# Performance work log

Hardware: AMD Instinct MI355X
Metric: run time of the kernel (lower is better)

The kernel has to match this reference:

```python
import jax, jax.numpy as jnp
import numpy as np

B, S, D = 4, 2048, 1024
H = 16
DK = D // H  # 64


def setup_inputs() -> dict:
    key = jax.random.key(0)
    k1, k2, k3 = jax.random.split(key, 3)
    std_qkv = (2.0 / (D + 3 * D)) ** 0.5
    std_o = (2.0 / (D + D)) ** 0.5
    x = jax.random.normal(k1, (B, S, D), dtype=jnp.float32)
    W_qkv = jax.random.normal(k2, (3 * D, D), dtype=jnp.float32) * std_qkv
    W_o = jax.random.normal(k3, (D, D), dtype=jnp.float32) * std_o
    return {"x": x, "W_qkv": W_qkv, "W_o": W_o}


def reference(x, W_qkv, W_o):
    b, s, d = x.shape
    # qkv projection: [b, s, 3*H*DK]
    qkv = jnp.einsum('bsd,ed->bse', x, W_qkv)
    # rearrange '(c h dk)' -> c, b, h, s, dk
    qkv = qkv.reshape(b, s, 3, H, DK)
    qkv = jnp.transpose(qkv, (2, 0, 3, 1, 4))  # [3, b, h, s, dk]
    q, k, v = qkv[0], qkv[1], qkv[2]
    # scaled dot product attention with causal mask
    scores = jnp.einsum('bhqd,bhkd->bhqk', q, k) / (DK ** 0.5)
    causal = jnp.tril(jnp.ones((s, s), dtype=bool))
    scores = jnp.where(causal, scores, -jnp.inf)
    probs = jax.nn.softmax(scores, axis=-1)
    heads = jnp.einsum('bhqk,bhkd->bhqd', probs, v)
    # merge heads: [b, s, H*DK]
    heads = jnp.transpose(heads, (0, 2, 1, 3)).reshape(b, s, H * DK)
    return jnp.einsum('bse,de->bsd', heads, W_o)
```

## Files before the change

kernel.cpp:

```cpp
#include <hip/hip_runtime.h>
#include <hip/hip_bf16.h>

#define BB 4
#define SS 2048
#define DD 1024
#define HH 16
#define DKK 64

typedef __bf16 bf16x8 __attribute__((ext_vector_type(8)));
typedef float floatx4 __attribute__((ext_vector_type(4)));

#if __has_builtin(__builtin_amdgcn_exp2f)
#define EXP2(x) __builtin_amdgcn_exp2f(x)
#else
#define EXP2(x) exp2f(x)
#endif

__device__ __forceinline__ float b2f(unsigned short u) {
    union { unsigned int i; float f; } c;
    c.i = ((unsigned int)u) << 16;
    return c.f;
}
__device__ __forceinline__ unsigned short f2b(float f) {
    unsigned int i = __float_as_uint(f);
    unsigned int r = (i + 0x7FFFu + ((i >> 16) & 1u)) >> 16;
    return (unsigned short)r;
}

__device__ __forceinline__ void gload_lds16(const unsigned short* g,
                                            unsigned short* l) {
    __builtin_amdgcn_global_load_lds(
        (const __attribute__((address_space(1))) unsigned int*)g,
        (__attribute__((address_space(3))) unsigned int*)l, 16, 0, 0);
}

__global__ void cvt_f32_bf16(const float* __restrict__ in,
                             unsigned short* __restrict__ out, int n4) {
    int i = blockIdx.x * blockDim.x + threadIdx.x;
    if (i >= n4) return;
    float4 v = ((const float4*)in)[i];
    ushort4 o;
    o.x = f2b(v.x); o.y = f2b(v.y); o.z = f2b(v.z); o.w = f2b(v.w);
    ((ushort4*)out)[i] = o;
}

template <typename CT>
__global__ void gemm_nt_lds(const unsigned short* __restrict__ A,
                            const unsigned short* __restrict__ B,
                            CT* __restrict__ C, int M, int N, int K) {
    __shared__ unsigned short Alds[128][32];
    __shared__ unsigned short Blds[128][32];

    const int tid  = threadIdx.x;
    const int lane = tid & 63;
    const int w    = tid >> 6;
    const int wm   = (w & 1) * 64;
    const int wn   = (w >> 1) * 64;

    const int m0 = blockIdx.x * 128;
    const int n0 = blockIdx.y * 128;

    const int row16 = lane & 15;
    const int part  = lane >> 4;
    const int rbase = part * 4;

    const int srow = lane >> 2;
    const int scol = (lane & 3) * 8;

    const unsigned short* Ag = A + (size_t)(m0 + w * 16 + srow) * K + scol;
    const unsigned short* Bg = B + (size_t)(n0 + w * 16 + srow) * K + scol;
    unsigned short* Al = &Alds[w * 16][0];
    unsigned short* Bl = &Blds[w * 16][0];
    const size_t rstep = (size_t)64 * K;

    floatx4 acc[4][4] = {};

    for (int k0 = 0; k0 < K; k0 += 32) {
        __syncthreads();
        gload_lds16(Ag + k0,         Al);
        gload_lds16(Ag + rstep + k0, Al + 64 * 32);
        gload_lds16(Bg + k0,         Bl);
        gload_lds16(Bg + rstep + k0, Bl + 64 * 32);
        __syncthreads();

        bf16x8 af[4], bfr[4];
#pragma unroll
        for (int i = 0; i < 4; ++i)
            af[i] = *(const bf16x8*)&Alds[wm + i * 16 + row16][part * 8];
#pragma unroll
        for (int j = 0; j < 4; ++j)
            bfr[j] = *(const bf16x8*)&Blds[wn + j * 16 + row16][part * 8];
#pragma unroll
        for (int i = 0; i < 4; ++i)
#pragma unroll
            for (int j = 0; j < 4; ++j)
                acc[i][j] = __builtin_amdgcn_mfma_f32_16x16x32_bf16(
                    af[i], bfr[j], acc[i][j], 0, 0, 0);
    }

#pragma unroll
    for (int i = 0; i < 4; ++i) {
#pragma unroll
        for (int j = 0; j < 4; ++j) {
            const int row = m0 + wm + i * 16 + rbase;
            const int col = n0 + wn + j * 16 + row16;
#pragma unroll
            for (int r = 0; r < 4; ++r) {
                size_t idx = (size_t)(row + r) * N + col;
                if constexpr (sizeof(CT) == 2) C[idx] = f2b(acc[i][j][r]);
                else                           C[idx] = acc[i][j][r];
            }
        }
    }
}

__global__ void repack_kv(const unsigned short* __restrict__ qkv,
                          unsigned short* __restrict__ Kp,
                          unsigned short* __restrict__ Vt) {
    __shared__ unsigned short Vs[64][72];
    const int st = blockIdx.x, h = blockIdx.y, b = blockIdx.z;
    const int tid = threadIdx.x;
    const size_t base = ((size_t)((b * HH + h) * (SS / 64) + st)) * 4096;

#pragma unroll
    for (int p = 0; p < 2; ++p) {
        const int row = p * 32 + (tid >> 3);
        const int chunk = tid & 7;
        size_t src = (size_t)(b * SS + st * 64 + row) * (3 * DD) +
                     DD + h * DKK + chunk * 8;
        uint4 kv = *(const uint4*)(qkv + src);
        *(uint4*)(Kp + base + (chunk >> 2) * 2048 + row * 32 + (chunk & 3) * 8) = kv;
        uint4 vv = *(const uint4*)(qkv + src + DD);
        *(uint4*)&Vs[row][chunk * 8] = vv;
    }
    __syncthreads();
#pragma unroll
    for (int p = 0; p < 2; ++p) {
        const int dk = p * 32 + (tid >> 3);
        const int s8 = tid & 7;
        union { unsigned short u[8]; uint4 v; } pk;
#pragma unroll
        for (int j = 0; j < 8; ++j) pk.u[j] = Vs[s8 * 8 + j][dk];
        *(uint4*)(Vt + base + (s8 >> 2) * 2048 + dk * 32 + (s8 & 3) * 8) = pk.v;
    }
}

__global__ __launch_bounds__(256) void attn_mfma5(
    const unsigned short* __restrict__ qkv,
    const unsigned short* __restrict__ Kp,
    const unsigned short* __restrict__ Vt,
    unsigned short* __restrict__ heads) {
    const int tid  = threadIdx.x;
    const int lane = tid & 63;
    const int w    = tid >> 6;

    const int u0   = blockIdx.x;
    const int xcd  = u0 & 7;
    const int slot = u0 >> 3;
    const int pair = xcd * 8 + (slot >> 4);
    const int qx   = 15 - (slot & 15);
    const int b = pair >> 4, h = pair & 15;
    const int q0w = qx * 128 + w * 32;

    const int row16 = lane & 15;
    const int part  = lane >> 4;
    const int rbase = part * 4;
    const float c1 = 0.180336884f;

    bf16x8 qf[2][2];
#pragma unroll
    for (int qt = 0; qt < 2; ++qt)
#pragma unroll
        for (int u = 0; u < 2; ++u) {
            const unsigned short* qp = qkv +
                (size_t)(b * SS + q0w + qt * 16 + row16) * (3 * DD) +
                h * DKK + u * 32 + part * 8;
            union { uint4 r; unsigned short us[8]; } raw;
            raw.r = *(const uint4*)qp;
            union { unsigned short us[8]; bf16x8 v; } sq;
#pragma unroll
            for (int j = 0; j < 8; ++j) sq.us[j] = f2b(b2f(raw.us[j]) * c1);
            qf[qt][u] = sq.v;
        }

    floatx4 O[2][4] = {};
    float mrow[2] = {-1e30f, -1e30f}, lrow[2] = {0.f, 0.f};

    const size_t tb = (size_t)pair * (SS / 64) * 4096;
    const int ntiles = (q0w + 31) / 64 + 1;

    for (int t = 0; t < ntiles; ++t) {
        const int k0 = t * 64;
        const unsigned short* kbase = Kp + tb + (size_t)t * 4096;
        const unsigned short* vbase = Vt + tb + (size_t)t * 4096;
        bf16x8 kf[2][4], vf[2][4];
#pragma unroll
        for (int u = 0; u < 2; ++u)
#pragma unroll
            for (int i = 0; i < 4; ++i) {
                kf[u][i] = *(const bf16x8*)(kbase + u * 2048 +
                                            (i * 16 + row16) * 32 + part * 8);
                vf[u][i] = *(const bf16x8*)(vbase + u * 2048 +
                                            (i * 16 + row16) * 32 + part * 8);
            }

#pragma unroll
        for (int qt = 0; qt < 2; ++qt) {
            floatx4 sc[4] = {};
#pragma unroll
            for (int u = 0; u < 2; ++u)
#pragma unroll
                for (int kt = 0; kt < 4; ++kt)
                    sc[kt] = __builtin_amdgcn_mfma_f32_16x16x32_bf16(
                        kf[u][kt], qf[qt][u], sc[kt], 0, 0, 0);

            const int qa = q0w + qt * 16 + row16;
            const bool full = (k0 + 63 <= q0w + qt * 16);
            float mx = -1e30f;
#pragma unroll
            for (int kt = 0; kt < 4; ++kt)
#pragma unroll
                for (int r = 0; r < 4; ++r) {
                    float s = sc[kt][r];
                    if (!full) {
                        int ka = k0 + kt * 16 + rbase + r;
                        s = (ka <= qa) ? s : -1e30f;
                    }
                    sc[kt][r] = s;
                    mx = fmaxf(mx, s);
                }
            mx = fmaxf(mx, __shfl_xor(mx, 16));
            mx = fmaxf(mx, __shfl_xor(mx, 32));
            float mnew = fmaxf(mrow[qt], mx);
            float alpha = EXP2(mrow[qt] - mnew);

            float ps = 0.f;
            unsigned int pk[4][2];
#pragma unroll
            for (int kt = 0; kt < 4; ++kt) {
                float e0 = EXP2(sc[kt][0] - mnew);
                float e1 = EXP2(sc[kt][1] - mnew);
                float e2 = EXP2(sc[kt][2] - mnew);
                float e3 = EXP2(sc[kt][3] - mnew);
                ps += (e0 + e1) + (e2 + e3);
                pk[kt][0] = (unsigned int)f2b(e0) | ((unsigned int)f2b(e1) << 16);
                pk[kt][1] = (unsigned int)f2b(e2) | ((unsigned int)f2b(e3) << 16);
            }
            ps += __shfl_xor(ps, 16);
            ps += __shfl_xor(ps, 32);
            lrow[qt] = lrow[qt] * alpha + ps;
            mrow[qt] = mnew;

#pragma unroll
            for (int dt = 0; dt < 4; ++dt) O[qt][dt] *= alpha;

            const int l0 = row16 + ((part & 1) * 2 + 0) * 16;
            const int l1 = row16 + ((part & 1) * 2 + 1) * 16;
            const bool hi = (part >> 1);
#pragma unroll
            for (int u = 0; u < 2; ++u) {
                unsigned int lo00 = (unsigned int)__shfl((int)pk[2 * u][0], l0);
                unsigned int lo01 = (unsigned int)__shfl((int)pk[2 * u][1], l0);
                unsigned int lo10 = (unsigned int)__shfl((int)pk[2 * u][0], l1);
                unsigned int lo11 = (unsigned int)__shfl((int)pk[2 * u][1], l1);
                unsigned int hi00 = (unsigned int)__shfl((int)pk[2 * u + 1][0], l0);
                unsigned int hi01 = (unsigned int)__shfl((int)pk[2 * u + 1][1], l0);
                unsigned int hi10 = (unsigned int)__shfl((int)pk[2 * u + 1][0], l1);
                unsigned int hi11 = (unsigned int)__shfl((int)pk[2 * u + 1][1], l1);
                union { unsigned int u32[4]; bf16x8 v; } P;
                P.u32[0] = hi ? hi00 : lo00;
                P.u32[1] = hi ? hi01 : lo01;
                P.u32[2] = hi ? hi10 : lo10;
                P.u32[3] = hi ? hi11 : lo11;
#pragma unroll
                for (int dt = 0; dt < 4; ++dt)
                    O[qt][dt] = __builtin_amdgcn_mfma_f32_16x16x32_bf16(
                        vf[u][dt], P.v, O[qt][dt], 0, 0, 0);
            }
        }
    }

#pragma unroll
    for (int qt = 0; qt < 2; ++qt) {
        float inv = 1.f / lrow[qt];
#pragma unroll
        for (int dt = 0; dt < 4; ++dt) {
            ushort4 o4;
            o4.x = f2b(O[qt][dt][0] * inv);
            o4.y = f2b(O[qt][dt][1] * inv);
            o4.z = f2b(O[qt][dt][2] * inv);
            o4.w = f2b(O[qt][dt][3] * inv);
            size_t base = (size_t)(b * SS + q0w + qt * 16 + row16) * DD +
                          h * DKK + dt * 16 + rbase;
            *(ushort4*)&heads[base] = o4;
        }
    }
}

extern "C" void kernel_launch(void* const* d_in, const int* in_sizes, int n_in,
                              void* d_out, int out_size, void* d_ws,
                              size_t ws_size, hipStream_t stream) {
    const float* x    = (const float*)d_in[0];
    const float* Wqkv = (const float*)d_in[1];
    const float* Wo   = (const float*)d_in[2];
    float* out = (float*)d_out;

    const size_t NX  = (size_t)BB * SS * DD;
    const size_t NWQ = (size_t)3 * DD * DD;
    const size_t NWO = (size_t)DD * DD;
    const size_t NKV = (size_t)BB * HH * SS * DKK;

    unsigned short* xb     = (unsigned short*)d_ws;
    unsigned short* wqkvb  = xb + NX;
    unsigned short* wob    = wqkvb + NWQ;
    unsigned short* qkvb   = wob + NWO;
    unsigned short* headsb = qkvb + (size_t)BB * SS * 3 * DD;
    unsigned short* Kp     = headsb + NX;
    unsigned short* Vtp    = Kp + NKV;

    cvt_f32_bf16<<<(int)(NX / 4 / 256), 256, 0, stream>>>(x, xb, (int)(NX / 4));
    cvt_f32_bf16<<<(int)(NWQ / 4 / 256), 256, 0, stream>>>(Wqkv, wqkvb, (int)(NWQ / 4));
    cvt_f32_bf16<<<(int)(NWO / 4 / 256), 256, 0, stream>>>(Wo, wob, (int)(NWO / 4));

    gemm_nt_lds<unsigned short><<<dim3(BB * SS / 128, 3 * DD / 128), 256, 0,
                                  stream>>>(xb, wqkvb, qkvb, BB * SS, 3 * DD, DD);

    repack_kv<<<dim3(SS / 64, HH, BB), 256, 0, stream>>>(qkvb, Kp, Vtp);

    attn_mfma5<<<dim3(1024), 256, 0, stream>>>(qkvb, Kp, Vtp, headsb);

    gemm_nt_lds<float><<<dim3(BB * SS / 128, DD / 128), 256, 0, stream>>>(
        headsb, wob, out, BB * SS, DD, DD);
}
```

Baseline: 319.7 us.

## Pair complementary causal query strips per wave to balance work and share K/V loads

Each wave now processes two 32-row query strips, j and 63-j, so every wave does the same total number of causal key tiles. The K/V fragments loaded for each tile are shared by both strips, which roughly halves K/V global loads for the short strip. The grid is halved to 512 blocks with launch_bounds(256,2), and the bf16 packing switches to a cheaper round-half-up pkpair. The cost is higher register pressure from two live accumulator states, and the rounding differs slightly from round-to-nearest-even.

Result: faster. 269.7 us (-15.6%).

```diff
diff --git a/kernel.cpp b/kernel.cpp
--- a/kernel.cpp
+++ b/kernel.cpp
@@ -25,6 +25,11 @@
     unsigned int i = __float_as_uint(f);
     unsigned int r = (i + 0x7FFFu + ((i >> 16) & 1u)) >> 16;
     return (unsigned short)r;
+}
+__device__ __forceinline__ unsigned int pkpair(float a, float b) {
+    unsigned int ia = (__float_as_uint(a) + 0x8000u) >> 16;
+    unsigned int ib = (__float_as_uint(b) + 0x8000u) & 0xffff0000u;
+    return ia | ib;
 }
 
 __device__ __forceinline__ void gload_lds16(const unsigned short* g,
@@ -145,7 +150,139 @@
     }
 }
 
-__global__ __launch_bounds__(256) void attn_mfma5(
+struct StripState {
+    bf16x8 qf[2][2];
+    floatx4 O[2][4];
+    float mrow[2], lrow[2];
+    int q0w;
+};
+
+__device__ __forceinline__ void strip_init(
+    StripState& S, const unsigned short* __restrict__ qkv,
+    int b, int h, int q0w, int row16, int part) {
+    const float c1 = 0.180336884f;
+    S.q0w = q0w;
+#pragma unroll
+    for (int qt = 0; qt < 2; ++qt) {
+        S.mrow[qt] = -1e30f;
+        S.lrow[qt] = 0.f;
+#pragma unroll
+        for (int dt = 0; dt < 4; ++dt) S.O[qt][dt] = floatx4{0, 0, 0, 0};
+#pragma unroll
+        for (int u = 0; u < 2; ++u) {
+            const unsigned short* qp = qkv +
+                (size_t)(b * SS + q0w + qt * 16 + row16) * (3 * DD) +
+                h * DKK + u * 32 + part * 8;
+            union { uint4 r; unsigned short us[8]; } raw;
+            raw.r = *(const uint4*)qp;
+            union { unsigned short us[8]; bf16x8 v; } sq;
+#pragma unroll
+            for (int j = 0; j < 8; ++j) sq.us[j] = f2b(b2f(raw.us[j]) * c1);
+            S.qf[qt][u] = sq.v;
+        }
+    }
+}
+
+__device__ __forceinline__ void strip_tile(
+    StripState& S, int k0, const bf16x8 kf[2][4], const bf16x8 vf[2][4],
+    int row16, int part, int rbase) {
+#pragma unroll
+    for (int qt = 0; qt < 2; ++qt) {
+        floatx4 sc[4] = {};
+#pragma unroll
+        for (int u = 0; u < 2; ++u)
+#pragma unroll
+            for (int kt = 0; kt < 4; ++kt)
+                sc[kt] = __builtin_amdgcn_mfma_f32_16x16x32_bf16(
+                    kf[u][kt], S.qf[qt][u], sc[kt], 0, 0, 0);
+
+        const int qa = S.q0w + qt * 16 + row16;
+        const bool full = (k0 + 63 <= S.q0w + qt * 16);
+        float mx = -1e30f;
+#pragma unroll
+        for (int kt = 0; kt < 4; ++kt)
+#pragma unroll
+            for (int r = 0; r < 4; ++r) {
+                float s = sc[kt][r];
+                if (!full) {
+                    int ka = k0 + kt * 16 + rbase + r;
+                    s = (ka <= qa) ? s : -1e30f;
+                }
+                sc[kt][r] = s;
+                mx = fmaxf(mx, s);
+            }
+        mx = fmaxf(mx, __shfl_xor(mx, 16));
+        mx = fmaxf(mx, __shfl_xor(mx, 32));
+        float mnew = fmaxf(S.mrow[qt], mx);
+        float alpha = EXP2(S.mrow[qt] - mnew);
+
+        float ps = 0.f;
+        unsigned int pk[4][2];
+#pragma unroll
+        for (int kt = 0; kt < 4; ++kt) {
+            float e0 = EXP2(sc[kt][0] - mnew);
+            float e1 = EXP2(sc[kt][1] - mnew);
+            float e2 = EXP2(sc[kt][2] - mnew);
+            float e3 = EXP2(sc[kt][3] - mnew);
+            ps += (e0 + e1) + (e2 + e3);
+            pk[kt][0] = pkpair(e0, e1);
+            pk[kt][1] = pkpair(e2, e3);
+        }
+        ps += __shfl_xor(ps, 16);
+        ps += __shfl_xor(ps, 32);
+        S.lrow[qt] = S.lrow[qt] * alpha + ps;
+        S.mrow[qt] = mnew;
+
+#pragma unroll
+        for (int dt = 0; dt < 4; ++dt) S.O[qt][dt] *= alpha;
+
+        const int l0 = row16 + ((part & 1) * 2 + 0) * 16;
+        const int l1 = row16 + ((part & 1) * 2 + 1) * 16;
+        const bool hi = (part >> 1);
+#pragma unroll
+        for (int u = 0; u < 2; ++u) {
+            unsigned int lo00 = (unsigned int)__shfl((int)pk[2 * u][0], l0);
+            unsigned int lo01 = (unsigned int)__shfl((int)pk[2 * u][1], l0);
+            unsigned int lo10 = (unsigned int)__shfl((int)pk[2 * u][0], l1);
+            unsigned int lo11 = (unsigned int)__shfl((int)pk[2 * u][1], l1);
+            unsigned int hi00 = (unsigned int)__shfl((int)pk[2 * u + 1][0], l0);
+            unsigned int hi01 = (unsigned int)__shfl((int)pk[2 * u + 1][1], l0);
+            unsigned int hi10 = (unsigned int)__shfl((int)pk[2 * u + 1][0], l1);
+            unsigned int hi11 = (unsigned int)__shfl((int)pk[2 * u + 1][1], l1);
+            union { unsigned int u32[4]; bf16x8 v; } P;
+            P.u32[0] = hi ? hi00 : lo00;
+            P.u32[1] = hi ? hi01 : lo01;
+            P.u32[2] = hi ? hi10 : lo10;
+            P.u32[3] = hi ? hi11 : lo11;
+#pragma unroll
+            for (int dt = 0; dt < 4; ++dt)
+                S.O[qt][dt] = __builtin_amdgcn_mfma_f32_16x16x32_bf16(
+                    vf[u][dt], P.v, S.O[qt][dt], 0, 0, 0);
+        }
+    }
+}
+
+__device__ __forceinline__ void strip_store(
+    StripState& S, unsigned short* __restrict__ heads,
+    int b, int h, int row16, int rbase) {
+#pragma unroll
+    for (int qt = 0; qt < 2; ++qt) {
+        float inv = 1.f / S.lrow[qt];
+#pragma unroll
+        for (int dt = 0; dt < 4; ++dt) {
+            ushort4 o4;
+            o4.x = f2b(S.O[qt][dt][0] * inv);
+            o4.y = f2b(S.O[qt][dt][1] * inv);
+            o4.z = f2b(S.O[qt][dt][2] * inv);
+            o4.w = f2b(S.O[qt][dt][3] * inv);
+            size_t base = (size_t)(b * SS + S.q0w + qt * 16 + row16) * DD +
+                          h * DKK + dt * 16 + rbase;
+            *(ushort4*)&heads[base] = o4;
+        }
+    }
+}
+
+__global__ __launch_bounds__(256, 2) void attn_mfma6(
     const unsigned short* __restrict__ qkv,
     const unsigned short* __restrict__ Kp,
     const unsigned short* __restrict__ Vt,
@@ -154,42 +291,29 @@
     const int lane = tid & 63;
     const int w    = tid >> 6;
 
-    const int u0   = blockIdx.x;
-    const int xcd  = u0 & 7;
-    const int slot = u0 >> 3;
-    const int pair = xcd * 8 + (slot >> 4);
-    const int qx   = 15 - (slot & 15);
+    const int bx   = blockIdx.x;
+    const int xcd  = bx & 7;
+    const int slot = bx >> 3;
+    const int pair = xcd * 8 + (slot >> 3);
+    const int blk  = slot & 7;
     const int b = pair >> 4, h = pair & 15;
-    const int q0w = qx * 128 + w * 32;
+
+    const int jA = blk * 4 + w;
+    const int jB = 63 - jA;
+    const int ntA = jA / 2 + 1;
+    const int ntB = jB / 2 + 1;
 
     const int row16 = lane & 15;
     const int part  = lane >> 4;
     const int rbase = part * 4;
-    const float c1 = 0.180336884f;
-
-    bf16x8 qf[2][2];
-#pragma unroll
-    for (int qt = 0; qt < 2; ++qt)
-#pragma unroll
-        for (int u = 0; u < 2; ++u) {
-            const unsigned short* qp = qkv +
-                (size_t)(b * SS + q0w + qt * 16 + row16) * (3 * DD) +
-                h * DKK + u * 32 + part * 8;
-            union { uint4 r; unsigned short us[8]; } raw;
-            raw.r = *(const uint4*)qp;
-            union { unsigned short us[8]; bf16x8 v; } sq;
-#pragma unroll
-            for (int j = 0; j < 8; ++j) sq.us[j] = f2b(b2f(raw.us[j]) * c1);
-            qf[qt][u] = sq.v;
-        }
-
-    floatx4 O[2][4] = {};
-    float mrow[2] = {-1e30f, -1e30f}, lrow[2] = {0.f, 0.f};
+
+    StripState SA, SB;
+    strip_init(SA, qkv, b, h, jA * 32, row16, part);
+    strip_init(SB, qkv, b, h, jB * 32, row16, part);
 
     const size_t tb = (size_t)pair * (SS / 64) * 4096;
-    const int ntiles = (q0w + 31) / 64 + 1;
-
-    for (int t = 0; t < ntiles; ++t) {
+
+    for (int t = 0; t < ntB; ++t) {
         const int k0 = t * 64;
         const unsigned short* kbase = Kp + tb + (size_t)t * 4096;
         const unsigned short* vbase = Vt + tb + (size_t)t * 4096;
@@ -203,98 +327,12 @@
                 vf[u][i] = *(const bf16x8*)(vbase + u * 2048 +
                                             (i * 16 + row16) * 32 + part * 8);
             }
-
-#pragma unroll
-        for (int qt = 0; qt < 2; ++qt) {
-            floatx4 sc[4] = {};
-#pragma unroll
-            for (int u = 0; u < 2; ++u)
-#pragma unroll
-                for (int kt = 0; kt < 4; ++kt)
-                    sc[kt] = __builtin_amdgcn_mfma_f32_16x16x32_bf16(
-                        kf[u][kt], qf[qt][u], sc[kt], 0, 0, 0);
-
-            const int qa = q0w + qt * 16 + row16;
-            const bool full = (k0 + 63 <= q0w + qt * 16);
-            float mx = -1e30f;
-#pragma unroll
-            for (int kt = 0; kt < 4; ++kt)
-#pragma unroll
-                for (int r = 0; r < 4; ++r) {
-                    float s = sc[kt][r];
-                    if (!full) {
-                        int ka = k0 + kt * 16 + rbase + r;
-                        s = (ka <= qa) ? s : -1e30f;
-                    }
-                    sc[kt][r] = s;
-                    mx = fmaxf(mx, s);
-                }
-            mx = fmaxf(mx, __shfl_xor(mx, 16));
-            mx = fmaxf(mx, __shfl_xor(mx, 32));
-            float mnew = fmaxf(mrow[qt], mx);
-            float alpha = EXP2(mrow[qt] - mnew);
-
-            float ps = 0.f;
-            unsigned int pk[4][2];
-#pragma unroll
-            for (int kt = 0; kt < 4; ++kt) {
-                float e0 = EXP2(sc[kt][0] - mnew);
-                float e1 = EXP2(sc[kt][1] - mnew);
-                float e2 = EXP2(sc[kt][2] - mnew);
-                float e3 = EXP2(sc[kt][3] - mnew);
-                ps += (e0 + e1) + (e2 + e3);
-                pk[kt][0] = (unsigned int)f2b(e0) | ((unsigned int)f2b(e1) << 16);
-                pk[kt][1] = (unsigned int)f2b(e2) | ((unsigned int)f2b(e3) << 16);
-            }
-            ps += __shfl_xor(ps, 16);
-            ps += __shfl_xor(ps, 32);
-            lrow[qt] = lrow[qt] * alpha + ps;
-            mrow[qt] = mnew;
-
-#pragma unroll
-            for (int dt = 0; dt < 4; ++dt) O[qt][dt] *= alpha;
-
-            const int l0 = row16 + ((part & 1) * 2 + 0) * 16;
-            const int l1 = row16 + ((part & 1) * 2 + 1) * 16;
-            const bool hi = (part >> 1);
-#pragma unroll
-            for (int u = 0; u < 2; ++u) {
-                unsigned int lo00 = (unsigned int)__shfl((int)pk[2 * u][0], l0);
-                unsigned int lo01 = (unsigned int)__shfl((int)pk[2 * u][1], l0);
-                unsigned int lo10 = (unsigned int)__shfl((int)pk[2 * u][0], l1);
-                unsigned int lo11 = (unsigned int)__shfl((int)pk[2 * u][1], l1);
-                unsigned int hi00 = (unsigned int)__shfl((int)pk[2 * u + 1][0], l0);
-                unsigned int hi01 = (unsigned int)__shfl((int)pk[2 * u + 1][1], l0);
-                unsigned int hi10 = (unsigned int)__shfl((int)pk[2 * u + 1][0], l1);
-                unsigned int hi11 = (unsigned int)__shfl((int)pk[2 * u + 1][1], l1);
-                union { unsigned int u32[4]; bf16x8 v; } P;
-                P.u32[0] = hi ? hi00 : lo00;
-                P.u32[1] = hi ? hi01 : lo01;
-                P.u32[2] = hi ? hi10 : lo10;
-                P.u32[3] = hi ? hi11 : lo11;
-#pragma unroll
-                for (int dt = 0; dt < 4; ++dt)
-                    O[qt][dt] = __builtin_amdgcn_mfma_f32_16x16x32_bf16(
-                        vf[u][dt], P.v, O[qt][dt], 0, 0, 0);
-            }
-        }
-    }
-
-#pragma unroll
-    for (int qt = 0; qt < 2; ++qt) {
-        float inv = 1.f / lrow[qt];
-#pragma unroll
-        for (int dt = 0; dt < 4; ++dt) {
-            ushort4 o4;
-            o4.x = f2b(O[qt][dt][0] * inv);
-            o4.y = f2b(O[qt][dt][1] * inv);
-            o4.z = f2b(O[qt][dt][2] * inv);
-            o4.w = f2b(O[qt][dt][3] * inv);
-            size_t base = (size_t)(b * SS + q0w + qt * 16 + row16) * DD +
-                          h * DKK + dt * 16 + rbase;
-            *(ushort4*)&heads[base] = o4;
-        }
-    }
+        strip_tile(SB, k0, kf, vf, row16, part, rbase);
+        if (t < ntA) strip_tile(SA, k0, kf, vf, row16, part, rbase);
+    }
+
+    strip_store(SA, heads, b, h, row16, rbase);
+    strip_store(SB, heads, b, h, row16, rbase);
 }
 
 extern "C" void kernel_launch(void* const* d_in, const int* in_sizes, int n_in,
@@ -327,7 +365,7 @@
 
     repack_kv<<<dim3(SS / 64, HH, BB), 256, 0, stream>>>(qkvb, Kp, Vtp);
 
-    attn_mfma5<<<dim3(1024), 256, 0, stream>>>(qkvb, Kp, Vtp, headsb);
+    attn_mfma6<<<dim3(512), 256, 0, stream>>>(qkvb, Kp, Vtp, headsb);
 
     gemm_nt_lds<float><<<dim3(BB * SS / 128, DD / 128), 256, 0, stream>>>(
         headsb, wob, out, BB * SS, DD, DD);
```
